# Kernel tuning notes

Hardware: AMD Instinct MI355X
Metric: run time of the kernel (lower is better)

## Reference

```python
import jax, jax.numpy as jnp
import numpy as np


def setup_inputs() -> dict:
    key = jax.random.key(0)
    k1, k2, k3, k4, k5 = jax.random.split(key, 5)
    N, M, K = 200000, 50, 4
    T = 1000.0
    ti = jnp.sort(jax.random.uniform(k1, (N,), dtype=jnp.float32) * T)
    mi = jax.random.randint(k2, (N,), 0, M, dtype=jnp.int64)
    mu_at_events = jax.random.uniform(k3, (N,), dtype=jnp.float32) * 0.5 + 0.05
    alpha = jax.random.uniform(k4, (K, M, M), dtype=jnp.float32) * 0.1
    gamma = jax.random.uniform(k5, (K,), dtype=jnp.float32) * 2.0 + 0.5
    return {"ti": ti, "mi": mi, "mu_at_events": mu_at_events, "alpha": alpha, "gamma": gamma}


def _hawkes_logsum(ti, mi, mu_at_events, alpha, gamma):
    # ti: [N] sorted event times; mi: [N] event types in [0, M)
    # alpha: [K, M, M]; gamma: [K]; mu_at_events: [N]
    N = ti.shape[0]
    M = alpha.shape[1]
    # inter-event gaps; dt[0] = 0 so the first event has zero excitation state
    dt = jnp.concatenate([jnp.zeros((1,), ti.dtype), ti[1:] - ti[:-1]])  # [N]
    a = jnp.exp(-gamma[None, :] * dt[:, None])  # [N, K] decay factors
    # one-hot of the PREVIOUS event's type (row 0 is all-zero, matching e_mi)
    prev_onehot = jnp.zeros((N, M), ti.dtype).at[jnp.arange(1, N), mi[:-1]].set(1.0)
    b = a[:, None, :] * prev_onehot[:, :, None]  # [N, M, K]

    # linear recurrence S_i = a_i * S_{i-1} + b_i via associative scan
    # combine((a1,b1),(a2,b2)) = (a1*a2, a2*b1 + b2)
    def combine(x, y):
        a1, b1 = x
        a2, b2 = y
        return (a1 * a2, a2[:, None, :] * b1 + b2)

    _, S = jax.lax.associative_scan(combine, (a, b))  # S: [N, M, K]
    # S[i, m, k] = sum_{j < i, m_j = m} exp(-gamma_k (t_i - t_j))
    alpha_at = alpha[:, mi, :]  # [K, N, M] rows of alpha for each event's type
    lam = mu_at_events + jnp.einsum('knm,nmk,k->n', alpha_at, S, gamma)  # [N]
    return jnp.sum(jnp.log(lam))


def reference(ti, mi, mu_at_events, alpha, gamma):
    return _hawkes_logsum(ti, mi, mu_at_events, alpha, gamma)
```

## Files before the change

kernel.cpp:

```cpp
#include <hip/hip_runtime.h>

#define CHUNK 256
#define MM 50
#define KK 4
#define STATE (MM*KK)
#define ASTRIDE 51
#define SUP 32
#define NSMAX 26
#define NSUB 8
#define SUBSZ 32
#define GMAX 1024

__device__ int      g_ticket;
__device__ unsigned g_flag[GMAX];
__device__ unsigned g_sflag[64];
__device__ float    g_chunkB[GMAX * STATE];
__device__ float    g_superB[64 * STATE];

__device__ __forceinline__ unsigned short f2bf(float x) {
  unsigned u = __float_as_uint(x);
  u += 0x7fffu + ((u >> 16) & 1u);
  return (unsigned short)(u >> 16);
}

__device__ __forceinline__ void st_agent(float* p, float v) {
  __hip_atomic_store(p, v, __ATOMIC_RELAXED, __HIP_MEMORY_SCOPE_AGENT);
}
__device__ __forceinline__ float ld_agent(const float* p) {
  return __hip_atomic_load(p, __ATOMIC_RELAXED, __HIP_MEMORY_SCOPE_AGENT);
}

__global__ __launch_bounds__(512) void hawkes_fused(
    const float* __restrict__ ti, const int* __restrict__ mi,
    const float* __restrict__ mu, const float* __restrict__ alpha,
    const float* __restrict__ gamma, float* __restrict__ out, int N, int G) {
  int tid = threadIdx.x;
  __shared__ int vid_s;
  __shared__ unsigned P0[MM * ASTRIDE];
  __shared__ unsigned P1[MM * ASTRIDE];
  __shared__ __align__(16) float4 Fj[CHUNK];
  __shared__ int   cj[CHUNK];
  __shared__ __align__(16) float Q[NSUB][STATE];
  __shared__ float red8[8];
  __shared__ float teL[SUP];
  __shared__ float tlast[NSMAX];

  if (tid == 0) vid_s = atomicAdd(&g_ticket, 1);

  float gk0 = gamma[0], gk1 = gamma[1], gk2 = gamma[2], gk3 = gamma[3];

  for (int i = tid; i < NSUB * STATE; i += 512) ((float*)Q)[i] = 0.f;

  for (int idx = tid; idx < MM * MM; idx += 512) {
    int c = idx / MM, cp = idx - c * MM;
    float a0 = gk0 * alpha[idx];
    float a1 = gk1 * alpha[2500 + idx];
    float a2 = gk2 * alpha[5000 + idx];
    float a3 = gk3 * alpha[7500 + idx];
    P0[c * ASTRIDE + cp] = (unsigned)f2bf(a0) | ((unsigned)f2bf(a1) << 16);
    P1[c * ASTRIDE + cp] = (unsigned)f2bf(a2) | ((unsigned)f2bf(a3) << 16);
  }
  __syncthreads();

  int tkt = vid_s;
  int epoch = tkt / G;
  int g = tkt - epoch * G;
  unsigned DONE = (unsigned)epoch + 1u;
  int l = g * CHUNK;
  int r = min(N, l + CHUNK);
  int cnt = r - l;
  int sup = g / SUP;
  int g0 = sup * SUP;
  int e = tid >> 1;
  int h = tid & 1;

  if (tid < SUP) {
    int c = g0 + tid;
    if (c < G) teL[tid] = ti[min(N, (c + 1) * CHUNK) - 1];
  } else if (tid >= 64 && tid < 64 + NSMAX) {
    int s = tid - 64;
    if (s < sup) tlast[s] = ti[min(N, (s + 1) * SUP * CHUNK) - 1];
  }

  float t_ref = ti[(g == 0) ? 0 : (l - 1)];
  bool valid = false;
  int myc = 0;
  float4 myF = make_float4(0.f, 0.f, 0.f, 0.f);
  if (tid < CHUNK) {
    int j = l - 1 + tid;
    valid = (j >= 0) && (j <= r - 2);
    if (valid) {
      myc = mi[j];
      float tj = ti[j] - t_ref;
      myF = make_float4(__expf(gk0 * tj), __expf(gk1 * tj),
                        __expf(gk2 * tj), __expf(gk3 * tj));
    }
    cj[tid] = myc;
    Fj[tid] = myF;
  }
  __syncthreads();

  if (valid) {
    float* q = &Q[tid >> 5][myc * KK];
    atomicAdd(q + 0, myF.x); atomicAdd(q + 1, myF.y);
    atomicAdd(q + 2, myF.z); atomicAdd(q + 3, myF.w);
  }
  __syncthreads();

  float gk = (tid & 2) ? ((tid & 1) ? gk3 : gk2) : ((tid & 1) ? gk1 : gk0);
  float Bv = 0.f, t_end = 0.f;
  if (tid < STATE) {
    t_end = teL[g - g0];
    float tot = 0.f;
    #pragma unroll
    for (int q = 0; q < NSUB; ++q) tot += Q[q][tid];
    Bv = __expf(-gk * (t_end - t_ref)) * tot;
    st_agent(&g_chunkB[g * STATE + tid], Bv);
  }
  if (g == 0 && tid == 0) st_agent(out, 0.f);
  __syncthreads();
  if (tid == 0) {
    asm volatile("s_waitcnt vmcnt(0)" ::: "memory");
    __hip_atomic_store(&g_flag[g], DONE, __ATOMIC_RELAXED, __HIP_MEMORY_SCOPE_AGENT);
  }

  int nloc = g - g0;
  if (tid < nloc) {
    while (__hip_atomic_load(&g_flag[g0 + tid], __ATOMIC_RELAXED,
                             __HIP_MEMORY_SCOPE_AGENT) != DONE)
      __builtin_amdgcn_s_sleep(2);
  }
  __syncthreads();

  float S = 0.f;
  if (tid < STATE) {
    #pragma unroll 4
    for (int u = 0; u < nloc; ++u)
      S += __expf(-gk * (t_ref - teL[u])) * ld_agent(&g_chunkB[(g0 + u) * STATE + tid]);
  }

  bool closer = (nloc == SUP - 1) || (g == G - 1);
  if (closer) {
    if (tid < STATE)
      st_agent(&g_superB[sup * STATE + tid], __expf(-gk * (t_end - t_ref)) * S + Bv);
    __syncthreads();
    if (tid == 0) {
      asm volatile("s_waitcnt vmcnt(0)" ::: "memory");
      __hip_atomic_store(&g_sflag[sup], DONE, __ATOMIC_RELAXED, __HIP_MEMORY_SCOPE_AGENT);
    }
  }

  if (tid < sup) {
    while (__hip_atomic_load(&g_sflag[tid], __ATOMIC_RELAXED,
                             __HIP_MEMORY_SCOPE_AGENT) != DONE)
      __builtin_amdgcn_s_sleep(2);
  }
  __syncthreads();

  if (tid < STATE) {
    #pragma unroll 4
    for (int s = 0; s < sup; ++s)
      S += __expf(-gk * (t_ref - tlast[s])) * ld_agent(&g_superB[s * STATE + tid]);
    float run = S;
    #pragma unroll
    for (int q = 0; q < NSUB; ++q) {
      float tq = Q[q][tid];
      Q[q][tid] = run;
      run += tq;
    }
  }
  __syncthreads();

  float local = 0.f;
  {
    int c_n = (e < cnt) ? mi[l + e] : 0;
    int rowb = c_n * ASTRIDE;
    const float4* wb = (const float4*)&Q[e >> 5][0];
    float4 acc = make_float4(0.f, 0.f, 0.f, 0.f);
    if (e < cnt) {
      int mlo = h * 25, mhi = mlo + 25;
      #pragma unroll 5
      for (int m = mlo; m < mhi; ++m) {
        unsigned p0 = P0[rowb + m];
        unsigned p1 = P1[rowb + m];
        float4 w = wb[m];
        acc.x += __uint_as_float(p0 << 16)         * w.x;
        acc.y += __uint_as_float(p0 & 0xffff0000u) * w.y;
        acc.z += __uint_as_float(p1 << 16)         * w.z;
        acc.w += __uint_as_float(p1 & 0xffff0000u) * w.w;
      }
      #pragma unroll 4
      for (int s = (e & ~(SUBSZ - 1)) + h; s <= e; s += 2) {
        unsigned p0 = P0[rowb + cj[s]];
        unsigned p1 = P1[rowb + cj[s]];
        float4 f = Fj[s];
        acc.x += __uint_as_float(p0 << 16)         * f.x;
        acc.y += __uint_as_float(p0 & 0xffff0000u) * f.y;
        acc.z += __uint_as_float(p1 << 16)         * f.z;
        acc.w += __uint_as_float(p1 & 0xffff0000u) * f.w;
      }
    }
    acc.x += __shfl_xor(acc.x, 1, 64);
    acc.y += __shfl_xor(acc.y, 1, 64);
    acc.z += __shfl_xor(acc.z, 1, 64);
    acc.w += __shfl_xor(acc.w, 1, 64);
    if (h == 0 && e < cnt) {
      float tn = ti[l + e] - t_ref;
      float lam = mu[l + e]
                + __expf(-gk0 * tn) * acc.x + __expf(-gk1 * tn) * acc.y
                + __expf(-gk2 * tn) * acc.z + __expf(-gk3 * tn) * acc.w;
      local = __logf(lam);
    }
  }
  #pragma unroll
  for (int off = 32; off > 0; off >>= 1)
    local += __shfl_down(local, off, 64);
  if ((tid & 63) == 0) red8[tid >> 6] = local;
  __syncthreads();
  if (tid == 0) {
    float acc8 = 0.f;
    #pragma unroll
    for (int w = 0; w < 8; ++w) acc8 += red8[w];
    atomicAdd(out, acc8);
  }
}

extern "C" void kernel_launch(void* const* d_in, const int* in_sizes, int n_in,
                              void* d_out, int out_size, void* d_ws, size_t ws_size,
                              hipStream_t stream) {
  const float* ti    = (const float*)d_in[0];
  const int*   mi    = (const int*)d_in[1];
  const float* mu    = (const float*)d_in[2];
  const float* alpha = (const float*)d_in[3];
  const float* gamma = (const float*)d_in[4];
  float* out = (float*)d_out;
  int N = in_sizes[0];
  int G = (N + CHUNK - 1) / CHUNK;
  if (G > GMAX) return;

  hawkes_fused<<<G, 512, 0, stream>>>(ti, mi, mu, alpha, gamma, out, N, G);
}
```

Measured before the change: 96.27 us.

## Overlap intra-chunk event contributions with cross-chunk prefix wait

```diff
diff --git a/kernel.cpp b/kernel.cpp
--- a/kernel.cpp
+++ b/kernel.cpp
@@ -22,6 +22,8 @@
   u += 0x7fffu + ((u >> 16) & 1u);
   return (unsigned short)(u >> 16);
 }
+__device__ __forceinline__ float bflo(unsigned u) { return __uint_as_float(u << 16); }
+__device__ __forceinline__ float bfhi(unsigned u) { return __uint_as_float(u & 0xffff0000u); }
 
 __device__ __forceinline__ void st_agent(float* p, float v) {
   __hip_atomic_store(p, v, __ATOMIC_RELAXED, __HIP_MEMORY_SCOPE_AGENT);
@@ -36,36 +38,19 @@
     const float* __restrict__ gamma, float* __restrict__ out, int N, int G) {
   int tid = threadIdx.x;
   __shared__ int vid_s;
-  __shared__ unsigned P0[MM * ASTRIDE];
-  __shared__ unsigned P1[MM * ASTRIDE];
+  __shared__ uint2 P[MM * ASTRIDE];
   __shared__ __align__(16) float4 Fj[CHUNK];
   __shared__ int   cj[CHUNK];
   __shared__ __align__(16) float Q[NSUB][STATE];
   __shared__ float red8[8];
   __shared__ float teL[SUP];
   __shared__ float tlast[NSMAX];
+  __shared__ float S_lds[STATE];
+  __shared__ __align__(16) float R_lds[MM * 20];
 
   if (tid == 0) vid_s = atomicAdd(&g_ticket, 1);
 
-  float gk0 = gamma[0], gk1 = gamma[1], gk2 = gamma[2], gk3 = gamma[3];
-
-  for (int i = tid; i < NSUB * STATE; i += 512) ((float*)Q)[i] = 0.f;
-
-  for (int idx = tid; idx < MM * MM; idx += 512) {
-    int c = idx / MM, cp = idx - c * MM;
-    float a0 = gk0 * alpha[idx];
-    float a1 = gk1 * alpha[2500 + idx];
-    float a2 = gk2 * alpha[5000 + idx];
-    float a3 = gk3 * alpha[7500 + idx];
-    P0[c * ASTRIDE + cp] = (unsigned)f2bf(a0) | ((unsigned)f2bf(a1) << 16);
-    P1[c * ASTRIDE + cp] = (unsigned)f2bf(a2) | ((unsigned)f2bf(a3) << 16);
-  }
-  __syncthreads();
-
-  int tkt = vid_s;
-  int epoch = tkt / G;
-  int g = tkt - epoch * G;
-  unsigned DONE = (unsigned)epoch + 1u;
+  int g = blockIdx.x;
   int l = g * CHUNK;
   int r = min(N, l + CHUNK);
   int cnt = r - l;
@@ -73,6 +58,10 @@
   int g0 = sup * SUP;
   int e = tid >> 1;
   int h = tid & 1;
+
+  float gk0 = gamma[0], gk1 = gamma[1], gk2 = gamma[2], gk3 = gamma[3];
+
+  for (int i = tid; i < NSUB * STATE; i += 512) ((float*)Q)[i] = 0.f;
 
   if (tid < SUP) {
     int c = g0 + tid;
@@ -116,52 +105,7 @@
     for (int q = 0; q < NSUB; ++q) tot += Q[q][tid];
     Bv = __expf(-gk * (t_end - t_ref)) * tot;
     st_agent(&g_chunkB[g * STATE + tid], Bv);
-  }
-  if (g == 0 && tid == 0) st_agent(out, 0.f);
-  __syncthreads();
-  if (tid == 0) {
-    asm volatile("s_waitcnt vmcnt(0)" ::: "memory");
-    __hip_atomic_store(&g_flag[g], DONE, __ATOMIC_RELAXED, __HIP_MEMORY_SCOPE_AGENT);
-  }
-
-  int nloc = g - g0;
-  if (tid < nloc) {
-    while (__hip_atomic_load(&g_flag[g0 + tid], __ATOMIC_RELAXED,
-                             __HIP_MEMORY_SCOPE_AGENT) != DONE)
-      __builtin_amdgcn_s_sleep(2);
-  }
-  __syncthreads();
-
-  float S = 0.f;
-  if (tid < STATE) {
-    #pragma unroll 4
-    for (int u = 0; u < nloc; ++u)
-      S += __expf(-gk * (t_ref - teL[u])) * ld_agent(&g_chunkB[(g0 + u) * STATE + tid]);
-  }
-
-  bool closer = (nloc == SUP - 1) || (g == G - 1);
-  if (closer) {
-    if (tid < STATE)
-      st_agent(&g_superB[sup * STATE + tid], __expf(-gk * (t_end - t_ref)) * S + Bv);
-    __syncthreads();
-    if (tid == 0) {
-      asm volatile("s_waitcnt vmcnt(0)" ::: "memory");
-      __hip_atomic_store(&g_sflag[sup], DONE, __ATOMIC_RELAXED, __HIP_MEMORY_SCOPE_AGENT);
-    }
-  }
-
-  if (tid < sup) {
-    while (__hip_atomic_load(&g_sflag[tid], __ATOMIC_RELAXED,
-                             __HIP_MEMORY_SCOPE_AGENT) != DONE)
-      __builtin_amdgcn_s_sleep(2);
-  }
-  __syncthreads();
-
-  if (tid < STATE) {
-    #pragma unroll 4
-    for (int s = 0; s < sup; ++s)
-      S += __expf(-gk * (t_ref - tlast[s])) * ld_agent(&g_superB[s * STATE + tid]);
-    float run = S;
+    float run = 0.f;
     #pragma unroll
     for (int q = 0; q < NSUB; ++q) {
       float tq = Q[q][tid];
@@ -169,48 +113,129 @@
       run += tq;
     }
   }
-  __syncthreads();
-
-  float local = 0.f;
-  {
-    int c_n = (e < cnt) ? mi[l + e] : 0;
-    int rowb = c_n * ASTRIDE;
+  if (g == 0 && tid == 0) st_agent(out, 0.f);
+
+  for (int idx = tid; idx < MM * MM; idx += 512) {
+    int c = idx / MM, cp = idx - c * MM;
+    float a0 = gk0 * alpha[idx];
+    float a1 = gk1 * alpha[2500 + idx];
+    float a2 = gk2 * alpha[5000 + idx];
+    float a3 = gk3 * alpha[7500 + idx];
+    P[c * ASTRIDE + cp] =
+        make_uint2((unsigned)f2bf(a0) | ((unsigned)f2bf(a1) << 16),
+                   (unsigned)f2bf(a2) | ((unsigned)f2bf(a3) << 16));
+  }
+  __syncthreads();
+  unsigned DONE = (unsigned)(vid_s / G) + 1u;
+  if (tid == 0) {
+    asm volatile("s_waitcnt vmcnt(0)" ::: "memory");
+    __hip_atomic_store(&g_flag[g], DONE, __ATOMIC_RELAXED, __HIP_MEMORY_SCOPE_AGENT);
+  }
+
+  int nloc = g - g0;
+  bool closer = (nloc == SUP - 1) || (g == G - 1);
+  float S = 0.f;
+
+  if (closer) {
+    if (tid < nloc) {
+      while (__hip_atomic_load(&g_flag[g0 + tid], __ATOMIC_RELAXED,
+                               __HIP_MEMORY_SCOPE_AGENT) != DONE)
+        __builtin_amdgcn_s_sleep(2);
+    }
+    __syncthreads();
+    if (tid < STATE) {
+      #pragma unroll 8
+      for (int u = 0; u < nloc; ++u)
+        S += __expf(-gk * (t_ref - teL[u])) * ld_agent(&g_chunkB[(g0 + u) * STATE + tid]);
+      st_agent(&g_superB[sup * STATE + tid], __expf(-gk * (t_end - t_ref)) * S + Bv);
+    }
+    __syncthreads();
+    if (tid == 0) {
+      asm volatile("s_waitcnt vmcnt(0)" ::: "memory");
+      __hip_atomic_store(&g_sflag[sup], DONE, __ATOMIC_RELAXED, __HIP_MEMORY_SCOPE_AGENT);
+    }
+  }
+
+  int c_n = (e < cnt) ? mi[l + e] : 0;
+  int rowb = c_n * ASTRIDE;
+  float tn = 0.f, mun = 0.f;
+  if (h == 0 && e < cnt) { tn = ti[l + e] - t_ref; mun = mu[l + e]; }
+  float4 acc = make_float4(0.f, 0.f, 0.f, 0.f);
+  if (e < cnt) {
     const float4* wb = (const float4*)&Q[e >> 5][0];
-    float4 acc = make_float4(0.f, 0.f, 0.f, 0.f);
-    if (e < cnt) {
+    if (e >= SUBSZ) {
       int mlo = h * 25, mhi = mlo + 25;
       #pragma unroll 5
       for (int m = mlo; m < mhi; ++m) {
-        unsigned p0 = P0[rowb + m];
-        unsigned p1 = P1[rowb + m];
+        uint2 p = P[rowb + m];
         float4 w = wb[m];
-        acc.x += __uint_as_float(p0 << 16)         * w.x;
-        acc.y += __uint_as_float(p0 & 0xffff0000u) * w.y;
-        acc.z += __uint_as_float(p1 << 16)         * w.z;
-        acc.w += __uint_as_float(p1 & 0xffff0000u) * w.w;
+        acc.x += bflo(p.x) * w.x; acc.y += bfhi(p.x) * w.y;
+        acc.z += bflo(p.y) * w.z; acc.w += bfhi(p.y) * w.w;
       }
-      #pragma unroll 4
-      for (int s = (e & ~(SUBSZ - 1)) + h; s <= e; s += 2) {
-        unsigned p0 = P0[rowb + cj[s]];
-        unsigned p1 = P1[rowb + cj[s]];
-        float4 f = Fj[s];
-        acc.x += __uint_as_float(p0 << 16)         * f.x;
-        acc.y += __uint_as_float(p0 & 0xffff0000u) * f.y;
-        acc.z += __uint_as_float(p1 << 16)         * f.z;
-        acc.w += __uint_as_float(p1 & 0xffff0000u) * f.w;
-      }
-    }
-    acc.x += __shfl_xor(acc.x, 1, 64);
-    acc.y += __shfl_xor(acc.y, 1, 64);
-    acc.z += __shfl_xor(acc.z, 1, 64);
-    acc.w += __shfl_xor(acc.w, 1, 64);
-    if (h == 0 && e < cnt) {
-      float tn = ti[l + e] - t_ref;
-      float lam = mu[l + e]
-                + __expf(-gk0 * tn) * acc.x + __expf(-gk1 * tn) * acc.y
-                + __expf(-gk2 * tn) * acc.z + __expf(-gk3 * tn) * acc.w;
-      local = __logf(lam);
-    }
+    }
+    #pragma unroll 4
+    for (int s = (e & ~(SUBSZ - 1)) + h; s <= e; s += 2) {
+      uint2 p = P[rowb + cj[s]];
+      float4 f = Fj[s];
+      acc.x += bflo(p.x) * f.x; acc.y += bfhi(p.x) * f.y;
+      acc.z += bflo(p.y) * f.z; acc.w += bfhi(p.y) * f.w;
+    }
+  }
+  acc.x += __shfl_xor(acc.x, 1, 64);
+  acc.y += __shfl_xor(acc.y, 1, 64);
+  acc.z += __shfl_xor(acc.z, 1, 64);
+  acc.w += __shfl_xor(acc.w, 1, 64);
+
+  if (!closer) {
+    if (tid < nloc) {
+      while (__hip_atomic_load(&g_flag[g0 + tid], __ATOMIC_RELAXED,
+                               __HIP_MEMORY_SCOPE_AGENT) != DONE)
+        __builtin_amdgcn_s_sleep(2);
+    }
+    __syncthreads();
+    if (tid < STATE) {
+      #pragma unroll 8
+      for (int u = 0; u < nloc; ++u)
+        S += __expf(-gk * (t_ref - teL[u])) * ld_agent(&g_chunkB[(g0 + u) * STATE + tid]);
+    }
+  }
+  if (tid < sup) {
+    while (__hip_atomic_load(&g_sflag[tid], __ATOMIC_RELAXED,
+                             __HIP_MEMORY_SCOPE_AGENT) != DONE)
+      __builtin_amdgcn_s_sleep(2);
+  }
+  __syncthreads();
+  if (tid < STATE) {
+    #pragma unroll 8
+    for (int s = 0; s < sup; ++s)
+      S += __expf(-gk * (t_ref - tlast[s])) * ld_agent(&g_superB[s * STATE + tid]);
+    S_lds[tid] = S;
+  }
+  __syncthreads();
+
+  if (tid < STATE) {
+    int c = tid >> 2, k = tid & 3;
+    float rv = 0.f;
+    #pragma unroll 5
+    for (int m = 0; m < MM; ++m) {
+      uint2 p = P[c * ASTRIDE + m];
+      unsigned w = (k & 2) ? p.y : p.x;
+      float pv = (k & 1) ? bfhi(w) : bflo(w);
+      rv += pv * S_lds[m * KK + k];
+    }
+    R_lds[c * 20 + k] = rv;
+  }
+  __syncthreads();
+
+  float local = 0.f;
+  if (h == 0 && e < cnt) {
+    float4 rv = *(const float4*)&R_lds[c_n * 20];
+    float lam = mun
+              + __expf(-gk0 * tn) * (acc.x + rv.x)
+              + __expf(-gk1 * tn) * (acc.y + rv.y)
+              + __expf(-gk2 * tn) * (acc.z + rv.z)
+              + __expf(-gk3 * tn) * (acc.w + rv.w);
+    local = __logf(lam);
   }
   #pragma unroll
   for (int off = 32; off > 0; off >>= 1)
```

Result: faster. 94.00 us (-2.4%).
